# Kernel tuning notes

Hardware: AMD Instinct MI355X
Metric: run time of the kernel (lower is better)

## Reference

```python
import jax, jax.numpy as jnp
import numpy as np

N_NODES = 50000
NUM_FEATS = 512
HIDDEN = 128
NUM_LAYERS = 4
NUM_CLASSES = 40
N_EDGES = 800000
ALPHA = 0.1
C_MIN = 0.2
RESIDUAL_WEIGHT = C_MIN - ALPHA  # 0.1
BIAS_SRELU = -10.0


def setup_inputs() -> dict:
    key = jax.random.key(0)
    ks = jax.random.split(key, 8)
    x = jax.random.normal(ks[0], (N_NODES, NUM_FEATS), dtype=jnp.float32)
    edge_index = jax.random.randint(ks[1], (2, N_EDGES), 0, N_NODES, dtype=jnp.int64)
    W_in = jax.random.normal(ks[2], (NUM_FEATS, HIDDEN), dtype=jnp.float32) / np.sqrt(NUM_FEATS)
    b_in = jnp.zeros((HIDDEN,), dtype=jnp.float32)
    W_layers = jax.random.normal(ks[3], (NUM_LAYERS, HIDDEN, HIDDEN), dtype=jnp.float32) / np.sqrt(HIDDEN)
    srelu_bias = jnp.full((NUM_LAYERS, HIDDEN), BIAS_SRELU, dtype=jnp.float32)
    W_out = jax.random.normal(ks[4], (HIDDEN, NUM_CLASSES), dtype=jnp.float32) / np.sqrt(HIDDEN)
    b_out = jnp.zeros((NUM_CLASSES,), dtype=jnp.float32)
    return {"x": x, "edge_index": edge_index, "W_in": W_in, "b_in": b_in,
            "W_layers": W_layers, "srelu_bias": srelu_bias,
            "W_out": W_out, "b_out": b_out}


def _gcn_norm(edge_index, n):
    # PyG gcn_norm: add self-loops, symmetric normalization D^-1/2 A D^-1/2
    loop = jnp.arange(n, dtype=edge_index.dtype)
    src = jnp.concatenate([edge_index[0], loop])
    dst = jnp.concatenate([edge_index[1], loop])
    ones = jnp.ones(src.shape[0], dtype=jnp.float32)
    deg = jax.ops.segment_sum(ones, dst, num_segments=n)
    dinv = jnp.where(deg > 0, jax.lax.rsqrt(deg), 0.0)
    norm = dinv[src] * dinv[dst]  # [E+N]
    return src, dst, norm


def reference(x, edge_index, W_in, b_in, W_layers, srelu_bias, W_out, b_out):
    n = x.shape[0]
    src, dst, norm = _gcn_norm(edge_index, n)

    # input layer (eval mode: dropout is identity), non-arxiv path
    h = jax.nn.relu(x @ W_in + b_in)
    x0 = h  # original_x residual anchor

    def layer(h, params):
        W, sb = params
        # sparse gather-scale-scatter aggregation: [E, H] messages
        agg = jax.ops.segment_sum(norm[:, None] * h[src], dst, num_segments=n)
        out = (1.0 - ALPHA - RESIDUAL_WEIGHT) * agg + RESIDUAL_WEIGHT * h + ALPHA * x0
        out = out @ W
        out = jax.nn.relu(out - sb) + sb  # SReLU
        return out, None

    h, _ = jax.lax.scan(layer, h, (W_layers, srelu_bias))
    return h @ W_out + b_out
```

## Files before the change

### kernel.cpp

```cpp
#include <hip/hip_runtime.h>
#include <hip/hip_fp16.h>

#define N_NODES 50000
#define E_EDGES 800000
#define F_IN 512
#define HID 128
#define N_LAYERS 4
#define C_OUT 40
#define SCAN_BLOCKS 196

typedef __attribute__((ext_vector_type(8))) short bf16x8;
typedef __attribute__((ext_vector_type(4))) float f32x4;

#define MFMA16(a, b, c) __builtin_amdgcn_mfma_f32_16x16x32_bf16(a, b, c, 0, 0, 0)

__device__ __forceinline__ void split2(float a, unsigned short& hi, unsigned short& lo) {
    unsigned u = __float_as_uint(a);
    unsigned r = u + 0x7FFFu + ((u >> 16) & 1u);
    hi = (unsigned short)(r >> 16);
    float hf = __uint_as_float(((unsigned)hi) << 16);
    lo = (unsigned short)(__float_as_uint(a - hf) >> 16);
}

__device__ __forceinline__ void async16(void* lds, const void* g) {
    __builtin_amdgcn_global_load_lds(
        (const __attribute__((address_space(1))) unsigned*)g,
        (__attribute__((address_space(3))) unsigned*)lds, 16, 0, 0);
}

__global__ void indeg_count(const int* __restrict__ ei, int* __restrict__ indeg) {
    int e = blockIdx.x * 256 + threadIdx.x;
    if (e < E_EDGES) {
        unsigned d = (unsigned)ei[E_EDGES + e];
        if (d < N_NODES) atomicAdd(&indeg[d], 1);
    }
}

__global__ void scan_p1(const int* __restrict__ indeg, int* __restrict__ bsum,
                        float* __restrict__ dinv) {
    __shared__ int red[4];
    int i = blockIdx.x * 256 + threadIdx.x;
    int v = (i < N_NODES) ? indeg[i] : 0;
    if (i < N_NODES) dinv[i] = rsqrtf(1.0f + (float)v);
    int s = v;
    #pragma unroll
    for (int off = 32; off > 0; off >>= 1) s += __shfl_down(s, off, 64);
    if ((threadIdx.x & 63) == 0) red[threadIdx.x >> 6] = s;
    __syncthreads();
    if (threadIdx.x == 0) bsum[blockIdx.x] = red[0] + red[1] + red[2] + red[3];
}

__launch_bounds__(256)
__global__ void scan_p2(const int* __restrict__ bsum, int* __restrict__ boff,
                        int* __restrict__ rowptr) {
    __shared__ int s[256];
    int t = threadIdx.x;
    int v = (t < SCAN_BLOCKS) ? bsum[t] : 0;
    s[t] = v;
    __syncthreads();
    #pragma unroll
    for (int off = 1; off < 256; off <<= 1) {
        int a = s[t];
        int b = (t >= off) ? s[t - off] : 0;
        __syncthreads();
        s[t] = a + b;
        __syncthreads();
    }
    if (t < SCAN_BLOCKS) boff[t] = (t == 0) ? 0 : s[t - 1];
    if (t == 255) rowptr[N_NODES] = s[SCAN_BLOCKS - 1];
}

__launch_bounds__(256)
__global__ void scan_p3(const int* __restrict__ indeg, const int* __restrict__ boff,
                        int* __restrict__ rowptr, int* __restrict__ cursor) {
    __shared__ int s[256];
    int t = threadIdx.x;
    int i = blockIdx.x * 256 + t;
    int v = (i < N_NODES) ? indeg[i] : 0;
    s[t] = v;
    __syncthreads();
    #pragma unroll
    for (int off = 1; off < 256; off <<= 1) {
        int a = s[t];
        int b = (t >= off) ? s[t - off] : 0;
        __syncthreads();
        s[t] = a + b;
        __syncthreads();
    }
    if (i < N_NODES) {
        int excl = boff[blockIdx.x] + s[t] - v;
        rowptr[i] = excl;
        cursor[i] = excl;
    }
}

__global__ void csr_fill(const int* __restrict__ ei, int* __restrict__ cursor,
                         int* __restrict__ csr) {
    int e = blockIdx.x * 256 + threadIdx.x;
    if (e < E_EDGES) {
        unsigned s = (unsigned)ei[e];
        unsigned d = (unsigned)ei[E_EDGES + e];
        if (s < N_NODES && d < N_NODES) {
            int pos = atomicAdd(&cursor[d], 1);
            csr[pos] = (int)s;
        }
    }
}

__global__ void wprep(const float* __restrict__ Wi, const float* __restrict__ Wl,
                      const float* __restrict__ Wo,
                      unsigned short* __restrict__ Wth, unsigned short* __restrict__ Wtl,
                      unsigned short* __restrict__ Wlth, unsigned short* __restrict__ Wltl,
                      unsigned short* __restrict__ Woth, unsigned short* __restrict__ Wotl) {
    int idx = blockIdx.x * 256 + threadIdx.x;
    unsigned short hi, lo;
    if (idx < F_IN * HID) {
        int k = idx >> 7, n = idx & 127;
        split2(Wi[idx], hi, lo);
        Wth[(size_t)n * F_IN + k] = hi;
        Wtl[(size_t)n * F_IN + k] = lo;
    } else if (idx < 2 * F_IN * HID) {
        int j = idx - F_IN * HID;
        int l = j >> 14, rem = j & 16383;
        int k = rem >> 7, n = rem & 127;
        split2(Wl[j], hi, lo);
        Wlth[(size_t)l * HID * HID + n * HID + k] = hi;
        Wltl[(size_t)l * HID * HID + n * HID + k] = lo;
    } else if (idx < 2 * F_IN * HID + 48 * HID) {
        int j = idx - 2 * F_IN * HID;
        int n = j >> 7, k = j & 127;
        float w = (n < C_OUT) ? Wo[(size_t)k * C_OUT + n] : 0.f;
        split2(w, hi, lo);
        Woth[(size_t)n * HID + k] = hi;
        Wotl[(size_t)n * HID + k] = lo;
    }
}

__launch_bounds__(256)
__global__ void gemm_in_mfma(const float* __restrict__ x,
                             const unsigned short* __restrict__ Bth,
                             const unsigned short* __restrict__ Btl,
                             const float* __restrict__ bi,
                             const float* __restrict__ dinv,
                             float* __restrict__ x0out,
                             __half* __restrict__ g16) {
    __shared__ __align__(16) unsigned short Ah[64 * 32];
    __shared__ __align__(16) unsigned short Al[64 * 32];
    __shared__ __align__(16) unsigned short Bh[128 * 32];
    __shared__ __align__(16) unsigned short Bl[128 * 32];
    const int t = threadIdx.x;
    const int lane = t & 63;
    const int wv = t >> 6;
    const int wr = wv >> 1, wc = wv & 1;
    const int row0 = blockIdx.x * 64;
    const int fr = lane & 15;
    const int fkg = lane >> 4;

    f32x4 acc[2][4] = {};

    for (int step = 0; step < 16; step++) {
        const int k0 = step * 32;
        #pragma unroll
        for (int i = 0; i < 2; i++) {
            int g = t + i * 256;
            int n = g >> 2, kg = g & 3;
            int kgp = kg ^ ((n >> 1) & 3);
            size_t src = (size_t)n * F_IN + k0 + kgp * 8;
            async16(&Bh[g * 8], &Bth[src]);
            async16(&Bl[g * 8], &Btl[src]);
        }
        #pragma unroll
        for (int i = 0; i < 2; i++) {
            int q = t + i * 256;
            int r = q >> 3, c4 = q & 7;
            int grow = row0 + r;
            float4 v = make_float4(0.f, 0.f, 0.f, 0.f);
            if (grow < N_NODES) v = *(const float4*)&x[(size_t)grow * F_IN + k0 + c4 * 4];
            ushort4 uh, ul;
            split2(v.x, uh.x, ul.x); split2(v.y, uh.y, ul.y);
            split2(v.z, uh.z, ul.z); split2(v.w, uh.w, ul.w);
            int gp = (c4 >> 1) ^ ((r >> 1) & 3);
            int idx = r * 32 + gp * 8 + (c4 & 1) * 4;
            *(ushort4*)&Ah[idx] = uh;
            *(ushort4*)&Al[idx] = ul;
        }
        __syncthreads();

        bf16x8 ah[2], al[2];
        #pragma unroll
        for (int mt = 0; mt < 2; mt++) {
            int arow = wr * 32 + mt * 16 + fr;
            int aidx = arow * 32 + (fkg ^ ((arow >> 1) & 3)) * 8;
            ah[mt] = *(bf16x8*)&Ah[aidx];
            al[mt] = *(bf16x8*)&Al[aidx];
        }
        #pragma unroll
        for (int nt = 0; nt < 4; nt++) {
            int n = wc * 64 + nt * 16 + fr;
            int bidx = n * 32 + (fkg ^ ((n >> 1) & 3)) * 8;
            bf16x8 bh = *(bf16x8*)&Bh[bidx];
            bf16x8 bl = *(bf16x8*)&Bl[bidx];
            #pragma unroll
            for (int mt = 0; mt < 2; mt++) {
                acc[mt][nt] = MFMA16(al[mt], bh, acc[mt][nt]);
                acc[mt][nt] = MFMA16(ah[mt], bl, acc[mt][nt]);
                acc[mt][nt] = MFMA16(ah[mt], bh, acc[mt][nt]);
            }
        }
        __syncthreads();
    }

    const int dcol = lane & 15;
    const int dr0 = (lane >> 4) * 4;
    float dv[2][4];
    #pragma unroll
    for (int mt = 0; mt < 2; mt++)
        #pragma unroll
        for (int j = 0; j < 4; j++) {
            int grow = row0 + wr * 32 + mt * 16 + dr0 + j;
            dv[mt][j] = (grow < N_NODES) ? dinv[grow] : 0.f;
        }
    #pragma unroll
    for (int nt = 0; nt < 4; nt++) {
        int gcol = wc * 64 + nt * 16 + dcol;
        float b = bi[gcol];
        #pragma unroll
        for (int mt = 0; mt < 2; mt++) {
            #pragma unroll
            for (int j = 0; j < 4; j++) {
                int grow = row0 + wr * 32 + mt * 16 + dr0 + j;
                if (grow < N_NODES) {
                    float v = fmaxf(acc[mt][nt][j] + b, 0.f);
                    x0out[(size_t)grow * HID + gcol] = v;
                    g16[(size_t)grow * HID + gcol] = __float2half(dv[mt][j] * v);
                }
            }
        }
    }
}

__launch_bounds__(256)
__global__ void aggregate(const int* __restrict__ rowptr, const int* __restrict__ csr,
                          const float* __restrict__ dinv,
                          const __half* __restrict__ g16,
                          const float* __restrict__ h, const float* __restrict__ x0,
                          float* __restrict__ comb) {
    const int node = blockIdx.x * 4 + (threadIdx.x >> 6);
    const int lane = threadIdx.x & 63;
    if (node >= N_NODES) return;

    const unsigned* g32 = (const unsigned*)g16;
    const float dd = dinv[node];
    const int beg = rowptr[node];
    const int end = rowptr[node + 1];

    float a0 = 0.f, a1 = 0.f, b0 = 0.f, b1 = 0.f;

    #define GACC(r, i) { \
        __half2 p = *(__half2*)&(r); \
        float2 f = __half22float2(p); \
        if ((i) & 1) { b0 += f.x; b1 += f.y; } else { a0 += f.x; a1 += f.y; } }

    int e = beg;
    for (; e + 16 <= end; e += 16) {
        unsigned r[16];
        #pragma unroll
        for (int i = 0; i < 16; i++) r[i] = g32[(size_t)csr[e + i] * 64 + lane];
        #pragma unroll
        for (int i = 0; i < 16; i++) GACC(r[i], i)
    }
    for (; e + 4 <= end; e += 4) {
        unsigned r[4];
        #pragma unroll
        for (int i = 0; i < 4; i++) r[i] = g32[(size_t)csr[e + i] * 64 + lane];
        #pragma unroll
        for (int i = 0; i < 4; i++) GACC(r[i], i)
    }
    for (; e < end; e++) {
        unsigned r = g32[(size_t)csr[e] * 64 + lane];
        GACC(r, 0)
    }
    #undef GACC

    float s0 = a0 + b0, s1 = a1 + b1;
    const float c1 = 0.8f * dd;
    const float c2 = 0.8f * dd * dd + 0.1f;
    float2 hv = ((const float2*)h)[(size_t)node * 64 + lane];
    float2 xv = ((const float2*)x0)[(size_t)node * 64 + lane];
    float2 o;
    o.x = fmaf(c1, s0, fmaf(c2, hv.x, 0.1f * xv.x));
    o.y = fmaf(c1, s1, fmaf(c2, hv.y, 0.1f * xv.y));
    ((float2*)comb)[(size_t)node * 64 + lane] = o;
}

__launch_bounds__(256)
__global__ void gemm_layer_mfma(const unsigned short* __restrict__ Bth,
                                const unsigned short* __restrict__ Btl,
                                const float* __restrict__ sb,
                                const float* __restrict__ dinv,
                                float* __restrict__ comb,
                                __half* __restrict__ g16) {
    __shared__ __align__(16) unsigned short Ah[64 * 128];
    __shared__ __align__(16) unsigned short Al[64 * 128];
    __shared__ __align__(16) unsigned short Bh[128 * 32];
    __shared__ __align__(16) unsigned short Bl[128 * 32];
    const int t = threadIdx.x;
    const int lane = t & 63;
    const int wv = t >> 6;
    const int wr = wv >> 1, wc = wv & 1;
    const int row0 = blockIdx.x * 64;
    const int fr = lane & 15;
    const int fkg = lane >> 4;

    f32x4 acc[2][4] = {};

    auto stageB = [&](int k0) {
        #pragma unroll
        for (int i = 0; i < 2; i++) {
            int g = t + i * 256;
            int n = g >> 2, kg = g & 3;
            int kgp = kg ^ ((n >> 1) & 3);
            size_t src = (size_t)n * HID + k0 + kgp * 8;
            async16(&Bh[g * 8], &Bth[src]);
            async16(&Bl[g * 8], &Btl[src]);
        }
    };

    stageB(0);
    #pragma unroll
    for (int i = 0; i < 8; i++) {
        int q = t + i * 256;
        int r = q >> 5, c4 = q & 31;
        int grow = row0 + r;
        float4 v = make_float4(0.f, 0.f, 0.f, 0.f);
        if (grow < N_NODES) v = *(const float4*)&comb[(size_t)grow * HID + c4 * 4];
        ushort4 uh, ul;
        split2(v.x, uh.x, ul.x); split2(v.y, uh.y, ul.y);
        split2(v.z, uh.z, ul.z); split2(v.w, uh.w, ul.w);
        int idx = (r * 128 + c4 * 4) ^ ((r & 7) << 3);
        *(ushort4*)&Ah[idx] = uh;
        *(ushort4*)&Al[idx] = ul;
    }
    __syncthreads();

    #pragma unroll
    for (int step = 0; step < 4; step++) {
        bf16x8 ah[2], al[2];
        #pragma unroll
        for (int mt = 0; mt < 2; mt++) {
            int arow = wr * 32 + mt * 16 + fr;
            int aidx = (arow * 128 + step * 32 + fkg * 8) ^ ((arow & 7) << 3);
            ah[mt] = *(bf16x8*)&Ah[aidx];
            al[mt] = *(bf16x8*)&Al[aidx];
        }
        #pragma unroll
        for (int nt = 0; nt < 4; nt++) {
            int n = wc * 64 + nt * 16 + fr;
            int bidx = n * 32 + (fkg ^ ((n >> 1) & 3)) * 8;
            bf16x8 bh = *(bf16x8*)&Bh[bidx];
            bf16x8 bl = *(bf16x8*)&Bl[bidx];
            #pragma unroll
            for (int mt = 0; mt < 2; mt++) {
                acc[mt][nt] = MFMA16(al[mt], bh, acc[mt][nt]);
                acc[mt][nt] = MFMA16(ah[mt], bl, acc[mt][nt]);
                acc[mt][nt] = MFMA16(ah[mt], bh, acc[mt][nt]);
            }
        }
        __syncthreads();
        if (step < 3) {
            stageB((step + 1) * 32);
            __syncthreads();
        }
    }

    const int dcol = lane & 15;
    const int dr0 = (lane >> 4) * 4;
    float dv[2][4];
    #pragma unroll
    for (int mt = 0; mt < 2; mt++)
        #pragma unroll
        for (int j = 0; j < 4; j++) {
            int grow = row0 + wr * 32 + mt * 16 + dr0 + j;
            dv[mt][j] = (grow < N_NODES) ? dinv[grow] : 0.f;
        }
    #pragma unroll
    for (int nt = 0; nt < 4; nt++) {
        int gcol = wc * 64 + nt * 16 + dcol;
        float s = sb[gcol];
        #pragma unroll
        for (int mt = 0; mt < 2; mt++) {
            #pragma unroll
            for (int j = 0; j < 4; j++) {
                int grow = row0 + wr * 32 + mt * 16 + dr0 + j;
                if (grow < N_NODES) {
                    float v = fmaxf(acc[mt][nt][j], s);
                    comb[(size_t)grow * HID + gcol] = v;
                    g16[(size_t)grow * HID + gcol] = __float2half(dv[mt][j] * v);
                }
            }
        }
    }
}

__launch_bounds__(256)
__global__ void gemm_layer_out(const unsigned short* __restrict__ Bth,
                               const unsigned short* __restrict__ Btl,
                               const float* __restrict__ sb,
                               const unsigned short* __restrict__ Woth,
                               const unsigned short* __restrict__ Wotl,
                               const float* __restrict__ bo,
                               const float* __restrict__ comb,
                               float* __restrict__ out) {
    __shared__ __align__(16) unsigned short Ah[64 * 128];
    __shared__ __align__(16) unsigned short Al[64 * 128];
    __shared__ __align__(16) unsigned short Bh[128 * 32];
    __shared__ __align__(16) unsigned short Bl[128 * 32];
    const int t = threadIdx.x;
    const int lane = t & 63;
    const int wv = t >> 6;
    const int wr = wv >> 1, wc = wv & 1;
    const int row0 = blockIdx.x * 64;
    const int fr = lane & 15;
    const int fkg = lane >> 4;

    f32x4 acc[2][4] = {};

    auto stageB = [&](int k0) {
        #pragma unroll
        for (int i = 0; i < 2; i++) {
            int g = t + i * 256;
            int n = g >> 2, kg = g & 3;
            int kgp = kg ^ ((n >> 1) & 3);
            size_t src = (size_t)n * HID + k0 + kgp * 8;
            async16(&Bh[g * 8], &Bth[src]);
            async16(&Bl[g * 8], &Btl[src]);
        }
    };

    stageB(0);
    #pragma unroll
    for (int i = 0; i < 8; i++) {
        int q = t + i * 256;
        int r = q >> 5, c4 = q & 31;
        int grow = row0 + r;
        float4 v = make_float4(0.f, 0.f, 0.f, 0.f);
        if (grow < N_NODES) v = *(const float4*)&comb[(size_t)grow * HID + c4 * 4];
        ushort4 uh, ul;
        split2(v.x, uh.x, ul.x); split2(v.y, uh.y, ul.y);
        split2(v.z, uh.z, ul.z); split2(v.w, uh.w, ul.w);
        int idx = (r * 128 + c4 * 4) ^ ((r & 7) << 3);
        *(ushort4*)&Ah[idx] = uh;
        *(ushort4*)&Al[idx] = ul;
    }
    __syncthreads();

    #pragma unroll
    for (int step = 0; step < 4; step++) {
        bf16x8 ah[2], al[2];
        #pragma unroll
        for (int mt = 0; mt < 2; mt++) {
            int arow = wr * 32 + mt * 16 + fr;
            int aidx = (arow * 128 + step * 32 + fkg * 8) ^ ((arow & 7) << 3);
            ah[mt] = *(bf16x8*)&Ah[aidx];
            al[mt] = *(bf16x8*)&Al[aidx];
        }
        #pragma unroll
        for (int nt = 0; nt < 4; nt++) {
            int n = wc * 64 + nt * 16 + fr;
            int bidx = n * 32 + (fkg ^ ((n >> 1) & 3)) * 8;
            bf16x8 bh = *(bf16x8*)&Bh[bidx];
            bf16x8 bl = *(bf16x8*)&Bl[bidx];
            #pragma unroll
            for (int mt = 0; mt < 2; mt++) {
                acc[mt][nt] = MFMA16(al[mt], bh, acc[mt][nt]);
                acc[mt][nt] = MFMA16(ah[mt], bl, acc[mt][nt]);
                acc[mt][nt] = MFMA16(ah[mt], bh, acc[mt][nt]);
            }
        }
        __syncthreads();
        if (step < 3) {
            stageB((step + 1) * 32);
            __syncthreads();
        }
    }

    const int dcol = lane & 15;
    const int dr0 = (lane >> 4) * 4;
    #pragma unroll
    for (int nt = 0; nt < 4; nt++) {
        int col = wc * 64 + nt * 16 + dcol;
        float s = sb[col];
        #pragma unroll
        for (int mt = 0; mt < 2; mt++) {
            #pragma unroll
            for (int j = 0; j < 4; j++) {
                int row = wr * 32 + mt * 16 + dr0 + j;
                float v = fmaxf(acc[mt][nt][j], s);
                unsigned short hi, lo;
                split2(v, hi, lo);
                int idx = (row * 128 + col) ^ ((row & 7) << 3);
                Ah[idx] = hi;
                Al[idx] = lo;
            }
        }
    }
    __syncthreads();

    f32x4 oacc[3] = {};
    #pragma unroll
    for (int kk = 0; kk < 4; kk++) {
        int arow = wv * 16 + fr;
        int aidx = (arow * 128 + kk * 32 + fkg * 8) ^ ((arow & 7) << 3);
        bf16x8 ah = *(bf16x8*)&Ah[aidx];
        bf16x8 al = *(bf16x8*)&Al[aidx];
        #pragma unroll
        for (int nt = 0; nt < 3; nt++) {
            size_t boff = (size_t)(nt * 16 + fr) * HID + kk * 32 + fkg * 8;
            bf16x8 bh = *(const bf16x8*)&Woth[boff];
            bf16x8 bl = *(const bf16x8*)&Wotl[boff];
            oacc[nt] = MFMA16(al, bh, oacc[nt]);
            oacc[nt] = MFMA16(ah, bl, oacc[nt]);
            oacc[nt] = MFMA16(ah, bh, oacc[nt]);
        }
    }
    #pragma unroll
    for (int nt = 0; nt < 3; nt++) {
        int gcol = nt * 16 + dcol;
        if (gcol < C_OUT) {
            float b = bo[gcol];
            #pragma unroll
            for (int j = 0; j < 4; j++) {
                int grow = row0 + wv * 16 + dr0 + j;
                if (grow < N_NODES)
                    out[(size_t)grow * C_OUT + gcol] = oacc[nt][j] + b;
            }
        }
    }
}

extern "C" void kernel_launch(void* const* d_in, const int* in_sizes, int n_in,
                              void* d_out, int out_size, void* d_ws, size_t ws_size,
                              hipStream_t stream) {
    const float* x   = (const float*)d_in[0];
    const int*   ei  = (const int*)d_in[1];
    const float* Wi  = (const float*)d_in[2];
    const float* bi  = (const float*)d_in[3];
    const float* Wls = (const float*)d_in[4];
    const float* sbs = (const float*)d_in[5];
    const float* Wo  = (const float*)d_in[6];
    const float* bo  = (const float*)d_in[7];
    float* out = (float*)d_out;

    float* dinv    = (float*)d_ws;
    int*   indeg   = (int*)(dinv + 50176);
    int*   rowptr  = indeg + 50176;
    int*   cursor  = rowptr + 50304;
    int*   bsum    = cursor + 50176;
    int*   boff    = bsum + 256;
    int*   csr     = boff + 256;
    unsigned short* Wth  = (unsigned short*)(csr + 800000);
    unsigned short* Wtl  = Wth + 65536;
    unsigned short* Wlth = Wtl + 65536;
    unsigned short* Wltl = Wlth + 65536;
    unsigned short* Woth = Wltl + 65536;
    unsigned short* Wotl = Woth + 6144;
    float* x0  = (float*)(Wotl + 6144);
    float* hB  = x0 + (size_t)N_NODES * HID;
    float* hC  = hB + (size_t)N_NODES * HID;
    __half* g16 = (__half*)(hC + (size_t)N_NODES * HID);

    const int edgeBlocks = (E_EDGES + 255) / 256;
    const int gemmBlocks = (N_NODES + 63) / 64;
    const int aggBlocks  = (N_NODES + 3) / 4;
    const int wprepBlocks = (2 * F_IN * HID + 48 * HID + 255) / 256;

    hipMemsetAsync(indeg, 0, N_NODES * sizeof(int), stream);
    indeg_count<<<edgeBlocks, 256, 0, stream>>>(ei, indeg);
    scan_p1<<<SCAN_BLOCKS, 256, 0, stream>>>(indeg, bsum, dinv);
    scan_p2<<<1, 256, 0, stream>>>(bsum, boff, rowptr);
    scan_p3<<<SCAN_BLOCKS, 256, 0, stream>>>(indeg, boff, rowptr, cursor);
    csr_fill<<<edgeBlocks, 256, 0, stream>>>(ei, cursor, csr);
    wprep<<<wprepBlocks, 256, 0, stream>>>(Wi, Wls, Wo, Wth, Wtl, Wlth, Wltl, Woth, Wotl);

    gemm_in_mfma<<<gemmBlocks, 256, 0, stream>>>(x, Wth, Wtl, bi, dinv, x0, g16);

    float* h = x0;
    for (int l = 0; l < N_LAYERS - 1; l++) {
        float* next = (l & 1) ? hC : hB;
        aggregate<<<aggBlocks, 256, 0, stream>>>(rowptr, csr, dinv, g16, h, x0, next);
        gemm_layer_mfma<<<gemmBlocks, 256, 0, stream>>>(Wlth + (size_t)l * HID * HID,
                                                        Wltl + (size_t)l * HID * HID,
                                                        sbs + (size_t)l * HID, dinv,
                                                        next, g16);
        h = next;
    }
    aggregate<<<aggBlocks, 256, 0, stream>>>(rowptr, csr, dinv, g16, h, x0, hC);
    gemm_layer_out<<<gemmBlocks, 256, 0, stream>>>(Wlth + (size_t)3 * HID * HID,
                                                   Wltl + (size_t)3 * HID * HID,
                                                   sbs + (size_t)3 * HID,
                                                   Woth, Wotl, bo, hC, out);
}
```

Before: 394.7 us.

## Precompute residual term in GEMM epilogue and async-load input x tile

The GEMM epilogues now write a combined residual term, (0.8*dinv^2+0.1)*h + 0.1*x0, so each aggregate pass reads one fp32 row instead of two (h and x0). The input GEMM also stages x through LDS as raw fp32 using async global-to-LDS loads with an XOR swizzle. The bf16 hi/lo split then happens when fragments are read from LDS rather than at store time. In exchange the GEMM epilogue reads x0 and writes an extra array, and the split work is repeated by the waves that share each A fragment.

New measurement: 418.5 us. 1.06x slower.

```diff
diff --git a/kernel.cpp b/kernel.cpp
--- a/kernel.cpp
+++ b/kernel.cpp
@@ -20,6 +20,17 @@
     hi = (unsigned short)(r >> 16);
     float hf = __uint_as_float(((unsigned)hi) << 16);
     lo = (unsigned short)(__float_as_uint(a - hf) >> 16);
+}
+
+__device__ __forceinline__ void splitfrag(float4 a, float4 b, bf16x8& h8, bf16x8& l8) {
+    unsigned short hh, ll;
+    float v[8] = {a.x, a.y, a.z, a.w, b.x, b.y, b.z, b.w};
+    #pragma unroll
+    for (int i = 0; i < 8; i++) {
+        split2(v[i], hh, ll);
+        h8[i] = (short)hh;
+        l8[i] = (short)ll;
+    }
 }
 
 __device__ __forceinline__ void async16(void* lds, const void* g) {
@@ -143,9 +154,9 @@
                              const float* __restrict__ bi,
                              const float* __restrict__ dinv,
                              float* __restrict__ x0out,
+                             float* __restrict__ res0,
                              __half* __restrict__ g16) {
-    __shared__ __align__(16) unsigned short Ah[64 * 32];
-    __shared__ __align__(16) unsigned short Al[64 * 32];
+    __shared__ __align__(16) float Af[64 * 32];
     __shared__ __align__(16) unsigned short Bh[128 * 32];
     __shared__ __align__(16) unsigned short Bl[128 * 32];
     const int t = threadIdx.x;
@@ -171,18 +182,13 @@
         }
         #pragma unroll
         for (int i = 0; i < 2; i++) {
-            int q = t + i * 256;
-            int r = q >> 3, c4 = q & 7;
+            int gi = t + i * 256;
+            int r = gi >> 3, g = gi & 7;
             int grow = row0 + r;
-            float4 v = make_float4(0.f, 0.f, 0.f, 0.f);
-            if (grow < N_NODES) v = *(const float4*)&x[(size_t)grow * F_IN + k0 + c4 * 4];
-            ushort4 uh, ul;
-            split2(v.x, uh.x, ul.x); split2(v.y, uh.y, ul.y);
-            split2(v.z, uh.z, ul.z); split2(v.w, uh.w, ul.w);
-            int gp = (c4 >> 1) ^ ((r >> 1) & 3);
-            int idx = r * 32 + gp * 8 + (c4 & 1) * 4;
-            *(ushort4*)&Ah[idx] = uh;
-            *(ushort4*)&Al[idx] = ul;
+            if (grow < N_NODES) {
+                int gp = g ^ (r & 7);
+                async16(&Af[gi * 4], &x[(size_t)grow * F_IN + k0 + gp * 4]);
+            }
         }
         __syncthreads();
 
@@ -190,9 +196,10 @@
         #pragma unroll
         for (int mt = 0; mt < 2; mt++) {
             int arow = wr * 32 + mt * 16 + fr;
-            int aidx = arow * 32 + (fkg ^ ((arow >> 1) & 3)) * 8;
-            ah[mt] = *(bf16x8*)&Ah[aidx];
-            al[mt] = *(bf16x8*)&Al[aidx];
+            int sw = arow & 7;
+            float4 fa = *(float4*)&Af[(arow * 8 + ((2 * fkg) ^ sw)) * 4];
+            float4 fb = *(float4*)&Af[(arow * 8 + ((2 * fkg + 1) ^ sw)) * 4];
+            splitfrag(fa, fb, ah[mt], al[mt]);
         }
         #pragma unroll
         for (int nt = 0; nt < 4; nt++) {
@@ -230,9 +237,12 @@
             for (int j = 0; j < 4; j++) {
                 int grow = row0 + wr * 32 + mt * 16 + dr0 + j;
                 if (grow < N_NODES) {
+                    float d = dv[mt][j];
                     float v = fmaxf(acc[mt][nt][j] + b, 0.f);
-                    x0out[(size_t)grow * HID + gcol] = v;
-                    g16[(size_t)grow * HID + gcol] = __float2half(dv[mt][j] * v);
+                    size_t off = (size_t)grow * HID + gcol;
+                    x0out[off] = v;
+                    res0[off] = (0.8f * d * d + 0.2f) * v;
+                    g16[off] = __float2half(d * v);
                 }
             }
         }
@@ -243,7 +253,7 @@
 __global__ void aggregate(const int* __restrict__ rowptr, const int* __restrict__ csr,
                           const float* __restrict__ dinv,
                           const __half* __restrict__ g16,
-                          const float* __restrict__ h, const float* __restrict__ x0,
+                          const float* __restrict__ res,
                           float* __restrict__ comb) {
     const int node = blockIdx.x * 4 + (threadIdx.x >> 6);
     const int lane = threadIdx.x & 63;
@@ -284,12 +294,10 @@
 
     float s0 = a0 + b0, s1 = a1 + b1;
     const float c1 = 0.8f * dd;
-    const float c2 = 0.8f * dd * dd + 0.1f;
-    float2 hv = ((const float2*)h)[(size_t)node * 64 + lane];
-    float2 xv = ((const float2*)x0)[(size_t)node * 64 + lane];
+    float2 rv = ((const float2*)res)[(size_t)node * 64 + lane];
     float2 o;
-    o.x = fmaf(c1, s0, fmaf(c2, hv.x, 0.1f * xv.x));
-    o.y = fmaf(c1, s1, fmaf(c2, hv.y, 0.1f * xv.y));
+    o.x = fmaf(c1, s0, rv.x);
+    o.y = fmaf(c1, s1, rv.y);
     ((float2*)comb)[(size_t)node * 64 + lane] = o;
 }
 
@@ -298,7 +306,9 @@
                                 const unsigned short* __restrict__ Btl,
                                 const float* __restrict__ sb,
                                 const float* __restrict__ dinv,
-                                float* __restrict__ comb,
+                                const float* __restrict__ comb,
+                                const float* __restrict__ x0,
+                                float* __restrict__ res,
                                 __half* __restrict__ g16) {
     __shared__ __align__(16) unsigned short Ah[64 * 128];
     __shared__ __align__(16) unsigned short Al[64 * 128];
@@ -393,9 +403,11 @@
             for (int j = 0; j < 4; j++) {
                 int grow = row0 + wr * 32 + mt * 16 + dr0 + j;
                 if (grow < N_NODES) {
+                    float d = dv[mt][j];
                     float v = fmaxf(acc[mt][nt][j], s);
-                    comb[(size_t)grow * HID + gcol] = v;
-                    g16[(size_t)grow * HID + gcol] = __float2half(dv[mt][j] * v);
+                    size_t off = (size_t)grow * HID + gcol;
+                    res[off] = fmaf(0.8f * d * d + 0.1f, v, 0.1f * x0[off]);
+                    g16[off] = __float2half(d * v);
                 }
             }
         }
@@ -564,10 +576,10 @@
     unsigned short* Wltl = Wlth + 65536;
     unsigned short* Woth = Wltl + 65536;
     unsigned short* Wotl = Woth + 6144;
-    float* x0  = (float*)(Wotl + 6144);
-    float* hB  = x0 + (size_t)N_NODES * HID;
-    float* hC  = hB + (size_t)N_NODES * HID;
-    __half* g16 = (__half*)(hC + (size_t)N_NODES * HID);
+    float* x0   = (float*)(Wotl + 6144);
+    float* res  = x0 + (size_t)N_NODES * HID;
+    float* comb = res + (size_t)N_NODES * HID;
+    __half* g16 = (__half*)(comb + (size_t)N_NODES * HID);
 
     const int edgeBlocks = (E_EDGES + 255) / 256;
     const int gemmBlocks = (N_NODES + 63) / 64;
@@ -582,21 +594,18 @@
     csr_fill<<<edgeBlocks, 256, 0, stream>>>(ei, cursor, csr);
     wprep<<<wprepBlocks, 256, 0, stream>>>(Wi, Wls, Wo, Wth, Wtl, Wlth, Wltl, Woth, Wotl);
 
-    gemm_in_mfma<<<gemmBlocks, 256, 0, stream>>>(x, Wth, Wtl, bi, dinv, x0, g16);
-
-    float* h = x0;
+    gemm_in_mfma<<<gemmBlocks, 256, 0, stream>>>(x, Wth, Wtl, bi, dinv, x0, res, g16);
+
     for (int l = 0; l < N_LAYERS - 1; l++) {
-        float* next = (l & 1) ? hC : hB;
-        aggregate<<<aggBlocks, 256, 0, stream>>>(rowptr, csr, dinv, g16, h, x0, next);
+        aggregate<<<aggBlocks, 256, 0, stream>>>(rowptr, csr, dinv, g16, res, comb);
         gemm_layer_mfma<<<gemmBlocks, 256, 0, stream>>>(Wlth + (size_t)l * HID * HID,
                                                         Wltl + (size_t)l * HID * HID,
                                                         sbs + (size_t)l * HID, dinv,
-                                                        next, g16);
-        h = next;
-    }
-    aggregate<<<aggBlocks, 256, 0, stream>>>(rowptr, csr, dinv, g16, h, x0, hC);
+                                                        comb, x0, res, g16);
+    }
+    aggregate<<<aggBlocks, 256, 0, stream>>>(rowptr, csr, dinv, g16, res, comb);
     gemm_layer_out<<<gemmBlocks, 256, 0, stream>>>(Wlth + (size_t)3 * HID * HID,
                                                    Wltl + (size_t)3 * HID * HID,
                                                    sbs + (size_t)3 * HID,
-                                                   Woth, Wotl, bo, hC, out);
-}
+                                                   Woth, Wotl, bo, comb, out);
+}
```
